# Optimization experiments

Measured on AMD Instinct MI355X. Metric: run time of the kernel, lower is better.

The kernel has to match this reference:

```python
import jax, jax.numpy as jnp
import numpy as np
from jax import lax

TRAJ_STEPS = 50  # output_dim=100 -> 50 (x,y) waypoints


def setup_inputs() -> dict:
    key = jax.random.key(0)
    ks = jax.random.split(key, 12)
    s = 0.05  # small init scale to keep gates out of saturation
    return {
        "x": jax.random.normal(ks[0], (32768, 256), jnp.float32),
        "W1": jax.random.normal(ks[1], (256, 64), jnp.float32) * s,
        "b1": jax.random.normal(ks[2], (64,), jnp.float32) * s,
        "W2": jax.random.normal(ks[3], (64, 64), jnp.float32) * s,
        "b2": jax.random.normal(ks[4], (64,), jnp.float32) * s,
        "Wih": jax.random.normal(ks[5], (2, 192), jnp.float32) * s,   # GRU input weights, gate order (r,z,n)
        "bih": jax.random.normal(ks[6], (192,), jnp.float32) * s,
        "Whh": jax.random.normal(ks[7], (64, 192), jnp.float32) * s,  # GRU hidden weights
        "bhh": jax.random.normal(ks[8], (192,), jnp.float32) * s,
        "Wout": jax.random.normal(ks[9], (64, 2), jnp.float32) * s,
        "bout": jax.random.normal(ks[10], (2,), jnp.float32) * s,
    }


def _forward(x, W1, b1, W2, b2, Wih, bih, Whh, bhh, Wout, bout):
    H = W2.shape[1]
    # backbone MLP -> initial hidden state
    z = jax.nn.relu(x @ W1 + b1)
    z = jax.nn.relu(z @ W2 + b2)  # [B, H]

    def step(carry, _):
        wp, h = carry                      # wp: [B,2] current waypoint, h: [B,H]
        gi = wp @ Wih + bih                # [B, 3H]
        gh = h @ Whh + bhh                 # [B, 3H]
        ir, iz, inn = gi[..., :H], gi[..., H:2 * H], gi[..., 2 * H:]
        hr, hz, hn = gh[..., :H], gh[..., H:2 * H], gh[..., 2 * H:]
        r = jax.nn.sigmoid(ir + hr)
        u = jax.nn.sigmoid(iz + hz)
        n = jnp.tanh(inn + r * hn)
        h_new = (1.0 - u) * n + u * h      # PyTorch GRUCell update
        dx = jax.nn.sigmoid(h_new @ Wout + bout)  # [B,2]
        wp_new = wp + dx                   # residual accumulation
        return (wp_new, h_new), wp_new

    wp0 = jnp.zeros(x.shape[:-1] + (2,), z.dtype)
    _, wps = lax.scan(step, (wp0, z), None, length=TRAJ_STEPS)  # [T, B, 2]
    wps = jnp.moveaxis(wps, 0, -2)                              # [B, T, 2]
    return wps.reshape(x.shape[:-1] + (2 * TRAJ_STEPS,))        # [B, 2T]


def reference(x, W1, b1, W2, b2, Wih, bih, Whh, bhh, Wout, bout):
    return _forward(x, W1, b1, W2, b2, Wih, bih, Whh, bhh, Wout, bout)
```

## Files before the change

kernel.cpp:

```cpp
#include <hip/hip_runtime.h>

#define TRAJ 50

typedef __attribute__((ext_vector_type(8))) short short8;
typedef __attribute__((ext_vector_type(4))) float f32x4;

#if defined(__has_builtin)
#if __has_builtin(__builtin_amdgcn_exp2f)
#define EXP2F(x) __builtin_amdgcn_exp2f(x)
#else
#define EXP2F(x) exp2f(x)
#endif
#if __has_builtin(__builtin_amdgcn_rcpf)
#define RCPF(x) __builtin_amdgcn_rcpf(x)
#else
#define RCPF(x) (1.0f/(x))
#endif
#else
#define EXP2F(x) exp2f(x)
#define RCPF(x) (1.0f/(x))
#endif

__device__ __forceinline__ float sigm(float x){
  return RCPF(1.0f + EXP2F(-1.44269504f * x));
}
__device__ __forceinline__ float tanh_(float x){
  return 1.0f - 2.0f * RCPF(1.0f + EXP2F(2.88539008f * x));
}
__device__ __forceinline__ unsigned short f2bf(float f){
  union { float f; unsigned u; } v; v.f = f;
  unsigned u = v.u;
  u += 0x7FFFu + ((u >> 16) & 1u);
  return (unsigned short)(u >> 16);
}
__device__ __forceinline__ unsigned pk(unsigned short a, unsigned short b){
  return (unsigned)a | ((unsigned)b << 16);
}

#define MFMA16(A,B,C) __builtin_amdgcn_mfma_f32_16x16x32_bf16((A),(B),(C),0,0,0)

__global__ __launch_bounds__(256, 2) void gru_actor_kernel(
    const float* __restrict__ x,
    const float* __restrict__ W1, const float* __restrict__ b1,
    const float* __restrict__ W2, const float* __restrict__ b2,
    const float* __restrict__ Wih, const float* __restrict__ bih,
    const float* __restrict__ Whh, const float* __restrict__ bhh,
    const float* __restrict__ Wout, const float* __restrict__ bout,
    float* __restrict__ out)
{
  __shared__ __align__(16) char sm_a[32768];
  __shared__ __align__(16) char sm_w[24576];
  __shared__ float sm_b1[64];
  __shared__ float sm_b2[64];

  const int t    = threadIdx.x;
  const int row0 = blockIdx.x * 64;
  const int w    = t >> 6;
  const int l    = t & 63;
  const int lr   = l & 15;
  const int lg   = l >> 4;
  const int wrow = w * 16;
  const int myrow = wrow + lr;
  const int swz  = (myrow & 7) << 4;

  {
    const float4* xg = (const float4*)(x + (size_t)row0 * 256);
    #pragma unroll
    for (int it = 0; it < 16; ++it){
      int fi = t + it * 256;
      float4 v = xg[fi];
      int e = fi * 4;
      int row = e >> 8, col = e & 255;
      unsigned p0 = pk(f2bf(v.x), f2bf(v.y));
      unsigned p1 = pk(f2bf(v.z), f2bf(v.w));
      *(uint2*)(sm_a + row * 512 + ((col * 2) ^ ((row & 7) << 4))) = make_uint2(p0, p1);
    }
  }
  for (int n = t; n < 8192; n += 256){
    int i = n & 63, kk = n >> 6;
    *(unsigned short*)(sm_w + i * 256 + ((kk * 2) ^ ((i & 7) << 4))) = f2bf(W1[kk * 64 + i]);
  }
  for (int n = t; n < 4096; n += 256){
    int i = n & 63, kk = n >> 6;
    *(unsigned short*)(sm_w + 16384 + i * 128 + ((kk * 2) ^ ((i & 7) << 4))) = f2bf(W2[kk * 64 + i]);
  }
  if (t < 64){ sm_b1[t] = b1[t]; sm_b2[t] = b2[t]; }
  __syncthreads();

  f32x4 accL[4];
  #pragma unroll
  for (int T = 0; T < 4; ++T){
    const float4 bv = *(const float4*)(sm_b1 + 16 * T + lg * 4);
    accL[T] = (f32x4){bv.x, bv.y, bv.z, bv.w};
  }
  #pragma unroll
  for (int kb = 0; kb < 4; ++kb){
    short8 B = *(const short8*)(sm_a + myrow * 512 + ((kb * 64 + lg * 16) ^ swz));
    #pragma unroll
    for (int T = 0; T < 4; ++T){
      int ai = 16 * T + lr;
      short8 A = *(const short8*)(sm_w + ai * 256 + ((kb * 64 + lg * 16) ^ ((ai & 7) << 4)));
      accL[T] = MFMA16(A, B, accL[T]);
    }
  }
  __syncthreads();
  for (int n = t; n < 8192; n += 256){
    int i = n & 63, kk = n >> 6;
    *(unsigned short*)(sm_w + i * 256 + ((kk * 2) ^ ((i & 7) << 4))) = f2bf(W1[(128 + kk) * 64 + i]);
  }
  __syncthreads();
  #pragma unroll
  for (int kb = 0; kb < 4; ++kb){
    short8 B = *(const short8*)(sm_a + myrow * 512 + (((kb + 4) * 64 + lg * 16) ^ swz));
    #pragma unroll
    for (int T = 0; T < 4; ++T){
      int ai = 16 * T + lr;
      short8 A = *(const short8*)(sm_w + ai * 256 + ((kb * 64 + lg * 16) ^ ((ai & 7) << 4)));
      accL[T] = MFMA16(A, B, accL[T]);
    }
  }
  __syncthreads();

  #pragma unroll
  for (int T = 0; T < 4; ++T){
    f32x4 a = accL[T];
    unsigned p0 = pk(f2bf(fmaxf(a[0],0.f)), f2bf(fmaxf(a[1],0.f)));
    unsigned p1 = pk(f2bf(fmaxf(a[2],0.f)), f2bf(fmaxf(a[3],0.f)));
    int ib = (16 * T + lg * 4) * 2;
    *(uint2*)(sm_a + myrow * 128 + (ib ^ swz)) = make_uint2(p0, p1);
  }
  f32x4 acc2[4];
  #pragma unroll
  for (int T = 0; T < 4; ++T){
    const float4 bv = *(const float4*)(sm_b2 + 16 * T + lg * 4);
    acc2[T] = (f32x4){bv.x, bv.y, bv.z, bv.w};
  }
  #pragma unroll
  for (int kb = 0; kb < 2; ++kb){
    short8 B = *(const short8*)(sm_a + myrow * 128 + ((kb * 64 + lg * 16) ^ swz));
    #pragma unroll
    for (int T = 0; T < 4; ++T){
      int ai = 16 * T + lr;
      short8 A = *(const short8*)(sm_w + 16384 + ai * 128 + ((kb * 64 + lg * 16) ^ ((ai & 7) << 4)));
      acc2[T] = MFMA16(A, B, acc2[T]);
    }
  }
  float h[16];
  #pragma unroll
  for (int T = 0; T < 4; ++T){
    f32x4 a = acc2[T];
    #pragma unroll
    for (int r = 0; r < 4; ++r) h[4*T+r] = fmaxf(a[r], 0.f);
    unsigned p0 = pk(f2bf(h[4*T+0]), f2bf(h[4*T+1]));
    unsigned p1 = pk(f2bf(h[4*T+2]), f2bf(h[4*T+3]));
    int ib = (16 * T + lg * 4) * 2;
    *(uint2*)(sm_a + myrow * 128 + (ib ^ swz)) = make_uint2(p0, p1);
  }
  __syncthreads();

  for (int n = t; n < 12288; n += 256){
    int kk = n / 192;
    int i  = n - kk * 192;
    *(unsigned short*)(sm_w + i * 128 + ((kk * 2) ^ ((i & 7) << 4))) = f2bf(Whh[kk * 192 + i]);
  }
  __syncthreads();

  short8 Ah[12][2];
  #pragma unroll
  for (int T = 0; T < 12; ++T){
    int i = 16 * T + lr;
    #pragma unroll
    for (int kb = 0; kb < 2; ++kb)
      Ah[T][kb] = *(const short8*)(sm_w + i * 128 + ((kb * 64 + lg * 16) ^ ((i & 7) << 4)));
  }
  short8 Ak2[16];
  #pragma unroll
  for (int T = 0; T < 16; ++T){
    short8 f = (short8){0,0,0,0,0,0,0,0};
    if (lg == 0){
      float v0 = 0.f, v1 = 0.f, v2 = 0.f;
      if (T < 8){ int i = 16*T + lr; v0 = Wih[i]; v1 = Wih[192 + i]; v2 = bih[i] + bhh[i]; }
      else if (T < 12){ int i = 16*T + lr; v2 = bhh[i]; }
      else { int i = 128 + 16*(T-12) + lr; v0 = Wih[i]; v1 = Wih[192 + i]; v2 = bih[i]; }
      f[0] = (short)f2bf(v0); f[1] = (short)f2bf(v1); f[2] = (short)f2bf(v2);
    }
    Ak2[T] = f;
  }
  short8 Aout[2];
  #pragma unroll
  for (int kb = 0; kb < 2; ++kb){
    short8 f = (short8){0,0,0,0,0,0,0,0};
    if (lr < 2){
      #pragma unroll
      for (int j = 0; j < 8; ++j){
        int k = kb * 32 + lg * 8 + j;
        f[j] = (short)f2bf(Wout[k * 2 + lr]);
      }
    }
    Aout[kb] = f;
  }
  const float bo0 = bout[0], bo1 = bout[1];

  float wp0 = 0.f, wp1 = 0.f;
  float* outp = out + (size_t)(row0 + myrow) * 100;

  short8 B0 = *(const short8*)(sm_a + myrow * 128 + ((lg * 16) ^ swz));
  short8 B1 = *(const short8*)(sm_a + myrow * 128 + ((64 + lg * 16) ^ swz));

  #pragma unroll 1
  for (int s = 0; s < TRAJ; ++s){
    short8 B2 = (short8){0,0,0,0,0,0,0,0};
    if (lg == 0){
      B2[0] = (short)f2bf(wp0);
      B2[1] = (short)f2bf(wp1);
      B2[2] = (short)0x3F80;
    }
    #pragma unroll
    for (int tq = 0; tq < 4; ++tq){
      f32x4 aR = (f32x4){0,0,0,0}, aU = (f32x4){0,0,0,0};
      f32x4 aN = (f32x4){0,0,0,0}, aI = (f32x4){0,0,0,0};
      aR = MFMA16(Ah[tq    ][0], B0, aR);
      aR = MFMA16(Ah[tq    ][1], B1, aR);
      aR = MFMA16(Ak2[tq    ],   B2, aR);
      aU = MFMA16(Ah[4 + tq][0], B0, aU);
      aU = MFMA16(Ah[4 + tq][1], B1, aU);
      aU = MFMA16(Ak2[4 + tq],   B2, aU);
      aN = MFMA16(Ah[8 + tq][0], B0, aN);
      aN = MFMA16(Ah[8 + tq][1], B1, aN);
      aN = MFMA16(Ak2[8 + tq],   B2, aN);
      aI = MFMA16(Ak2[12 + tq],  B2, aI);
      #pragma unroll
      for (int r = 0; r < 4; ++r){
        float rv = sigm(aR[r]);
        float uv = sigm(aU[r]);
        float nv = tanh_(aI[r] + rv * aN[r]);
        int idx = 4 * tq + r;
        h[idx] = (1.f - uv) * nv + uv * h[idx];
      }
      unsigned p0 = pk(f2bf(h[4*tq+0]), f2bf(h[4*tq+1]));
      unsigned p1 = pk(f2bf(h[4*tq+2]), f2bf(h[4*tq+3]));
      *(uint2*)(sm_a + myrow * 128 + (((16*tq + lg*4)*2) ^ swz)) = make_uint2(p0, p1);
    }
    short8 nB0 = *(const short8*)(sm_a + myrow * 128 + ((lg * 16) ^ swz));
    short8 nB1 = *(const short8*)(sm_a + myrow * 128 + ((64 + lg * 16) ^ swz));
    f32x4 aD = (f32x4){0,0,0,0};
    if (lg == 0){ aD[0] = bo0; aD[1] = bo1; }
    aD = MFMA16(Aout[0], nB0, aD);
    aD = MFMA16(Aout[1], nB1, aD);
    if (lg == 0){
      wp0 += sigm(aD[0]);
      wp1 += sigm(aD[1]);
      *(float2*)(outp + 2 * s) = make_float2(wp0, wp1);
    }
    B0 = nB0; B1 = nB1;
  }
}

extern "C" void kernel_launch(void* const* d_in, const int* in_sizes, int n_in,
                              void* d_out, int out_size, void* d_ws, size_t ws_size,
                              hipStream_t stream) {
  (void)n_in; (void)out_size; (void)d_ws; (void)ws_size;
  const float* x    = (const float*)d_in[0];
  const float* W1   = (const float*)d_in[1];
  const float* b1   = (const float*)d_in[2];
  const float* W2   = (const float*)d_in[3];
  const float* b2   = (const float*)d_in[4];
  const float* Wih  = (const float*)d_in[5];
  const float* bih  = (const float*)d_in[6];
  const float* Whh  = (const float*)d_in[7];
  const float* bhh  = (const float*)d_in[8];
  const float* Wout = (const float*)d_in[9];
  const float* bout = (const float*)d_in[10];
  float* out = (float*)d_out;

  int nrows = in_sizes[0] / 256;
  int grid  = nrows / 64;
  gru_actor_kernel<<<dim3(grid), dim3(256), 0, stream>>>(
      x, W1, b1, W2, b2, Wih, bih, Whh, bhh, Wout, bout, out);
}
```

Baseline: 121.7 us.

## Split GRU gate columns across wave pairs with double-buffered hidden state

Block size doubles to 512 threads and each pair of waves shares 16 rows, with each wave computing half of the hidden units. The hidden state is exchanged through a double-buffered LDS region, with a block barrier every step. The sigmoid and tanh scale factors are folded into the weights, and the two sigmoids share a single reciprocal. W1 is now staged whole in LDS instead of in two halves. The aim is to halve the per-wave serial MFMA and transcendental chain in the 50-step recurrence and to drop register pressure, at the cost of a __syncthreads per step and more LDS per block.

```diff
diff --git a/kernel.cpp b/kernel.cpp
--- a/kernel.cpp
+++ b/kernel.cpp
@@ -1,4 +1,5 @@
 #include <hip/hip_runtime.h>
+#include <hip/hip_bf16.h>
 
 #define TRAJ 50
 
@@ -21,12 +22,6 @@
 #define RCPF(x) (1.0f/(x))
 #endif
 
-__device__ __forceinline__ float sigm(float x){
-  return RCPF(1.0f + EXP2F(-1.44269504f * x));
-}
-__device__ __forceinline__ float tanh_(float x){
-  return 1.0f - 2.0f * RCPF(1.0f + EXP2F(2.88539008f * x));
-}
 __device__ __forceinline__ unsigned short f2bf(float f){
   union { float f; unsigned u; } v; v.f = f;
   unsigned u = v.u;
@@ -36,10 +31,23 @@
 __device__ __forceinline__ unsigned pk(unsigned short a, unsigned short b){
   return (unsigned)a | ((unsigned)b << 16);
 }
+__device__ __forceinline__ unsigned pkbf(float a, float b){
+  union { __hip_bfloat162 h; unsigned u; } c;
+  c.h = __float22bfloat162_rn(make_float2(a, b));
+  return c.u;
+}
+__device__ __forceinline__ short8 mkfrag(uint2 v){
+  union { unsigned u[4]; short8 s; } c;
+  c.u[0] = v.x; c.u[1] = v.y; c.u[2] = 0u; c.u[3] = 0u;
+  return c.s;
+}
 
 #define MFMA16(A,B,C) __builtin_amdgcn_mfma_f32_16x16x32_bf16((A),(B),(C),0,0,0)
 
-__global__ __launch_bounds__(256, 2) void gru_actor_kernel(
+#define SSC (-1.44269504f)
+#define TSC ( 2.88539008f)
+
+__global__ __launch_bounds__(512, 4) void gru_actor_kernel(
     const float* __restrict__ x,
     const float* __restrict__ W1, const float* __restrict__ b1,
     const float* __restrict__ W2, const float* __restrict__ b2,
@@ -48,209 +56,198 @@
     const float* __restrict__ Wout, const float* __restrict__ bout,
     float* __restrict__ out)
 {
-  __shared__ __align__(16) char sm_a[32768];
-  __shared__ __align__(16) char sm_w[24576];
+  __shared__ __align__(16) char sm_x[32768];
+  __shared__ __align__(16) char sm_w[32768];
+  __shared__ __align__(16) char sm_w2[8192];
+  __shared__ __align__(16) char sm_wo[2048];
   __shared__ float sm_b1[64];
   __shared__ float sm_b2[64];
 
   const int t    = threadIdx.x;
   const int row0 = blockIdx.x * 64;
   const int w    = t >> 6;
+  const int pair = w >> 1;
+  const int p    = w & 1;
   const int l    = t & 63;
   const int lr   = l & 15;
   const int lg   = l >> 4;
-  const int wrow = w * 16;
-  const int myrow = wrow + lr;
-  const int swz  = (myrow & 7) << 4;
+  const int myrow = pair * 16 + lr;
+  const int swz  = (lr & 7) << 4;
 
   {
     const float4* xg = (const float4*)(x + (size_t)row0 * 256);
     #pragma unroll
-    for (int it = 0; it < 16; ++it){
-      int fi = t + it * 256;
+    for (int it = 0; it < 8; ++it){
+      int fi = t + it * 512;
       float4 v = xg[fi];
-      int e = fi * 4;
-      int row = e >> 8, col = e & 255;
-      unsigned p0 = pk(f2bf(v.x), f2bf(v.y));
-      unsigned p1 = pk(f2bf(v.z), f2bf(v.w));
-      *(uint2*)(sm_a + row * 512 + ((col * 2) ^ ((row & 7) << 4))) = make_uint2(p0, p1);
-    }
-  }
-  for (int n = t; n < 8192; n += 256){
+      int e = fi * 4, row = e >> 8, col = e & 255;
+      *(uint2*)(sm_x + row * 512 + ((col * 2) ^ ((row & 7) << 4))) =
+          make_uint2(pkbf(v.x, v.y), pkbf(v.z, v.w));
+    }
+  }
+  for (int n = t; n < 16384; n += 512){
     int i = n & 63, kk = n >> 6;
-    *(unsigned short*)(sm_w + i * 256 + ((kk * 2) ^ ((i & 7) << 4))) = f2bf(W1[kk * 64 + i]);
-  }
-  for (int n = t; n < 4096; n += 256){
+    *(unsigned short*)(sm_w + i * 512 + ((kk * 2) ^ ((i & 7) << 4))) = f2bf(W1[kk * 64 + i]);
+  }
+  for (int n = t; n < 4096; n += 512){
     int i = n & 63, kk = n >> 6;
-    *(unsigned short*)(sm_w + 16384 + i * 128 + ((kk * 2) ^ ((i & 7) << 4))) = f2bf(W2[kk * 64 + i]);
+    *(unsigned short*)(sm_w2 + i * 128 + ((kk * 2) ^ ((i & 7) << 4))) = f2bf(W2[kk * 64 + i]);
+  }
+  for (int n = t; n < 1024; n += 512){
+    int row = n & 15, k = n >> 4;
+    float v = (row < 2) ? SSC * Wout[k * 2 + row] : 0.0f;
+    *(unsigned short*)(sm_wo + row * 128 + k * 2) = f2bf(v);
   }
   if (t < 64){ sm_b1[t] = b1[t]; sm_b2[t] = b2[t]; }
   __syncthreads();
 
-  f32x4 accL[4];
+  const int ar0 = 16 * (2 * p + 0) + lr;
+  const int ar1 = 16 * (2 * p + 1) + lr;
+  f32x4 accL0, accL1;
+  {
+    float4 bva = *(const float4*)(sm_b1 + 16 * (2 * p + 0) + lg * 4);
+    float4 bvb = *(const float4*)(sm_b1 + 16 * (2 * p + 1) + lg * 4);
+    accL0 = (f32x4){bva.x, bva.y, bva.z, bva.w};
+    accL1 = (f32x4){bvb.x, bvb.y, bvb.z, bvb.w};
+  }
   #pragma unroll
-  for (int T = 0; T < 4; ++T){
-    const float4 bv = *(const float4*)(sm_b1 + 16 * T + lg * 4);
-    accL[T] = (f32x4){bv.x, bv.y, bv.z, bv.w};
-  }
+  for (int kb = 0; kb < 8; ++kb){
+    short8 B  = *(const short8*)(sm_x + myrow * 512 + ((kb * 64 + lg * 16) ^ swz));
+    short8 Aa = *(const short8*)(sm_w + ar0 * 512 + ((kb * 64 + lg * 16) ^ swz));
+    short8 Ab = *(const short8*)(sm_w + ar1 * 512 + ((kb * 64 + lg * 16) ^ swz));
+    accL0 = MFMA16(Aa, B, accL0);
+    accL1 = MFMA16(Ab, B, accL1);
+  }
+  __syncthreads();
+
+  {
+    f32x4 a0 = accL0, a1 = accL1;
+    *(uint2*)(sm_x + myrow * 128 + ((64 * p + 0  + 8 * lg) ^ swz)) =
+        make_uint2(pkbf(fmaxf(a0[0],0.f), fmaxf(a0[1],0.f)), pkbf(fmaxf(a0[2],0.f), fmaxf(a0[3],0.f)));
+    *(uint2*)(sm_x + myrow * 128 + ((64 * p + 32 + 8 * lg) ^ swz)) =
+        make_uint2(pkbf(fmaxf(a1[0],0.f), fmaxf(a1[1],0.f)), pkbf(fmaxf(a1[2],0.f), fmaxf(a1[3],0.f)));
+  }
+  for (int n = t; n < 12288; n += 512){
+    int kk = n / 192, i = n - kk * 192;
+    float s = (i < 128) ? SSC : TSC;
+    *(unsigned short*)(sm_w + i * 128 + ((kk * 2) ^ ((i & 7) << 4))) = f2bf(s * Whh[kk * 192 + i]);
+  }
+  __syncthreads();
+
+  float h[8];
+  {
+    f32x4 acc20, acc21;
+    float4 bva = *(const float4*)(sm_b2 + 16 * (2 * p + 0) + lg * 4);
+    float4 bvb = *(const float4*)(sm_b2 + 16 * (2 * p + 1) + lg * 4);
+    acc20 = (f32x4){bva.x, bva.y, bva.z, bva.w};
+    acc21 = (f32x4){bvb.x, bvb.y, bvb.z, bvb.w};
+    #pragma unroll
+    for (int kb = 0; kb < 2; ++kb){
+      short8 B  = *(const short8*)(sm_x + myrow * 128 + ((kb * 64 + lg * 16) ^ swz));
+      short8 Aa = *(const short8*)(sm_w2 + ar0 * 128 + ((kb * 64 + lg * 16) ^ swz));
+      short8 Ab = *(const short8*)(sm_w2 + ar1 * 128 + ((kb * 64 + lg * 16) ^ swz));
+      acc20 = MFMA16(Aa, B, acc20);
+      acc21 = MFMA16(Ab, B, acc21);
+    }
+    #pragma unroll
+    for (int r = 0; r < 4; ++r){ h[r] = fmaxf(acc20[r], 0.f); h[4 + r] = fmaxf(acc21[r], 0.f); }
+    *(uint2*)(sm_x + 8192 + myrow * 128 + ((64 * p + 0  + 8 * lg) ^ swz)) =
+        make_uint2(pkbf(h[0], h[1]), pkbf(h[2], h[3]));
+    *(uint2*)(sm_x + 8192 + myrow * 128 + ((64 * p + 32 + 8 * lg) ^ swz)) =
+        make_uint2(pkbf(h[4], h[5]), pkbf(h[6], h[7]));
+  }
+
+  short8 Ah[3][2][2];
   #pragma unroll
-  for (int kb = 0; kb < 4; ++kb){
-    short8 B = *(const short8*)(sm_a + myrow * 512 + ((kb * 64 + lg * 16) ^ swz));
-    #pragma unroll
-    for (int T = 0; T < 4; ++T){
-      int ai = 16 * T + lr;
-      short8 A = *(const short8*)(sm_w + ai * 256 + ((kb * 64 + lg * 16) ^ ((ai & 7) << 4)));
-      accL[T] = MFMA16(A, B, accL[T]);
-    }
-  }
-  __syncthreads();
-  for (int n = t; n < 8192; n += 256){
-    int i = n & 63, kk = n >> 6;
-    *(unsigned short*)(sm_w + i * 256 + ((kk * 2) ^ ((i & 7) << 4))) = f2bf(W1[(128 + kk) * 64 + i]);
-  }
-  __syncthreads();
-  #pragma unroll
-  for (int kb = 0; kb < 4; ++kb){
-    short8 B = *(const short8*)(sm_a + myrow * 512 + (((kb + 4) * 64 + lg * 16) ^ swz));
-    #pragma unroll
-    for (int T = 0; T < 4; ++T){
-      int ai = 16 * T + lr;
-      short8 A = *(const short8*)(sm_w + ai * 256 + ((kb * 64 + lg * 16) ^ ((ai & 7) << 4)));
-      accL[T] = MFMA16(A, B, accL[T]);
-    }
-  }
-  __syncthreads();
-
-  #pragma unroll
-  for (int T = 0; T < 4; ++T){
-    f32x4 a = accL[T];
-    unsigned p0 = pk(f2bf(fmaxf(a[0],0.f)), f2bf(fmaxf(a[1],0.f)));
-    unsigned p1 = pk(f2bf(fmaxf(a[2],0.f)), f2bf(fmaxf(a[3],0.f)));
-    int ib = (16 * T + lg * 4) * 2;
-    *(uint2*)(sm_a + myrow * 128 + (ib ^ swz)) = make_uint2(p0, p1);
-  }
-  f32x4 acc2[4];
-  #pragma unroll
-  for (int T = 0; T < 4; ++T){
-    const float4 bv = *(const float4*)(sm_b2 + 16 * T + lg * 4);
-    acc2[T] = (f32x4){bv.x, bv.y, bv.z, bv.w};
-  }
-  #pragma unroll
-  for (int kb = 0; kb < 2; ++kb){
-    short8 B = *(const short8*)(sm_a + myrow * 128 + ((kb * 64 + lg * 16) ^ swz));
-    #pragma unroll
-    for (int T = 0; T < 4; ++T){
-      int ai = 16 * T + lr;
-      short8 A = *(const short8*)(sm_w + 16384 + ai * 128 + ((kb * 64 + lg * 16) ^ ((ai & 7) << 4)));
-      acc2[T] = MFMA16(A, B, acc2[T]);
-    }
-  }
-  float h[16];
-  #pragma unroll
-  for (int T = 0; T < 4; ++T){
-    f32x4 a = acc2[T];
-    #pragma unroll
-    for (int r = 0; r < 4; ++r) h[4*T+r] = fmaxf(a[r], 0.f);
-    unsigned p0 = pk(f2bf(h[4*T+0]), f2bf(h[4*T+1]));
-    unsigned p1 = pk(f2bf(h[4*T+2]), f2bf(h[4*T+3]));
-    int ib = (16 * T + lg * 4) * 2;
-    *(uint2*)(sm_a + myrow * 128 + (ib ^ swz)) = make_uint2(p0, p1);
-  }
-  __syncthreads();
-
-  for (int n = t; n < 12288; n += 256){
-    int kk = n / 192;
-    int i  = n - kk * 192;
-    *(unsigned short*)(sm_w + i * 128 + ((kk * 2) ^ ((i & 7) << 4))) = f2bf(Whh[kk * 192 + i]);
-  }
-  __syncthreads();
-
-  short8 Ah[12][2];
-  #pragma unroll
-  for (int T = 0; T < 12; ++T){
-    int i = 16 * T + lr;
-    #pragma unroll
-    for (int kb = 0; kb < 2; ++kb)
-      Ah[T][kb] = *(const short8*)(sm_w + i * 128 + ((kb * 64 + lg * 16) ^ ((i & 7) << 4)));
-  }
-  short8 Ak2[16];
-  #pragma unroll
-  for (int T = 0; T < 16; ++T){
-    short8 f = (short8){0,0,0,0,0,0,0,0};
-    if (lg == 0){
-      float v0 = 0.f, v1 = 0.f, v2 = 0.f;
-      if (T < 8){ int i = 16*T + lr; v0 = Wih[i]; v1 = Wih[192 + i]; v2 = bih[i] + bhh[i]; }
-      else if (T < 12){ int i = 16*T + lr; v2 = bhh[i]; }
-      else { int i = 128 + 16*(T-12) + lr; v0 = Wih[i]; v1 = Wih[192 + i]; v2 = bih[i]; }
-      f[0] = (short)f2bf(v0); f[1] = (short)f2bf(v1); f[2] = (short)f2bf(v2);
-    }
-    Ak2[T] = f;
-  }
-  short8 Aout[2];
-  #pragma unroll
-  for (int kb = 0; kb < 2; ++kb){
-    short8 f = (short8){0,0,0,0,0,0,0,0};
-    if (lr < 2){
+  for (int g = 0; g < 3; ++g){
+    #pragma unroll
+    for (int tql = 0; tql < 2; ++tql){
+      int i = g * 64 + 32 * p + 16 * tql + lr;
       #pragma unroll
-      for (int j = 0; j < 8; ++j){
-        int k = kb * 32 + lg * 8 + j;
-        f[j] = (short)f2bf(Wout[k * 2 + lr]);
-      }
-    }
-    Aout[kb] = f;
-  }
-  const float bo0 = bout[0], bo1 = bout[1];
+      for (int kb = 0; kb < 2; ++kb)
+        Ah[g][tql][kb] = *(const short8*)(sm_w + i * 128 + ((kb * 64 + lg * 16) ^ swz));
+    }
+  }
+  uint2 Ak2p[4][2] = {};
+  if (lg == 0){
+    #pragma unroll
+    for (int tql = 0; tql < 2; ++tql){
+      int dr = 32 * p + 16 * tql + lr;
+      int du = 64 + dr, dn = 128 + dr;
+      Ak2p[0][tql] = make_uint2(pk(f2bf(SSC*Wih[dr]), f2bf(SSC*Wih[192+dr])),
+                                pk(f2bf(SSC*(bih[dr]+bhh[dr])), 0));
+      Ak2p[1][tql] = make_uint2(pk(f2bf(SSC*Wih[du]), f2bf(SSC*Wih[192+du])),
+                                pk(f2bf(SSC*(bih[du]+bhh[du])), 0));
+      Ak2p[2][tql] = make_uint2(0u, pk(f2bf(TSC*bhh[dn]), 0));
+      Ak2p[3][tql] = make_uint2(pk(f2bf(TSC*Wih[dn]), f2bf(TSC*Wih[192+dn])),
+                                pk(f2bf(TSC*bih[dn]), 0));
+    }
+  }
+  const float bo0 = SSC * bout[0], bo1 = SSC * bout[1];
+  __syncthreads();
 
   float wp0 = 0.f, wp1 = 0.f;
   float* outp = out + (size_t)(row0 + myrow) * 100;
-
-  short8 B0 = *(const short8*)(sm_a + myrow * 128 + ((lg * 16) ^ swz));
-  short8 B1 = *(const short8*)(sm_a + myrow * 128 + ((64 + lg * 16) ^ swz));
+  short8 B0 = *(const short8*)(sm_x + 8192 + myrow * 128 + ((0  + lg * 16) ^ swz));
+  short8 B1 = *(const short8*)(sm_x + 8192 + myrow * 128 + ((64 + lg * 16) ^ swz));
 
   #pragma unroll 1
   for (int s = 0; s < TRAJ; ++s){
-    short8 B2 = (short8){0,0,0,0,0,0,0,0};
-    if (lg == 0){
-      B2[0] = (short)f2bf(wp0);
-      B2[1] = (short)f2bf(wp1);
-      B2[2] = (short)0x3F80;
-    }
-    #pragma unroll
-    for (int tq = 0; tq < 4; ++tq){
+    char* bufW = sm_x + ((s & 1) << 13);
+    short8 B2;
+    {
+      unsigned b2lo = 0u, b2hi = 0u;
+      if (lg == 0){ b2lo = pkbf(wp0, wp1); b2hi = 0x00003F80u; }
+      union { unsigned u[4]; short8 sv; } c;
+      c.u[0] = b2lo; c.u[1] = b2hi; c.u[2] = 0u; c.u[3] = 0u;
+      B2 = c.sv;
+    }
+    #pragma unroll
+    for (int tql = 0; tql < 2; ++tql){
       f32x4 aR = (f32x4){0,0,0,0}, aU = (f32x4){0,0,0,0};
       f32x4 aN = (f32x4){0,0,0,0}, aI = (f32x4){0,0,0,0};
-      aR = MFMA16(Ah[tq    ][0], B0, aR);
-      aR = MFMA16(Ah[tq    ][1], B1, aR);
-      aR = MFMA16(Ak2[tq    ],   B2, aR);
-      aU = MFMA16(Ah[4 + tq][0], B0, aU);
-      aU = MFMA16(Ah[4 + tq][1], B1, aU);
-      aU = MFMA16(Ak2[4 + tq],   B2, aU);
-      aN = MFMA16(Ah[8 + tq][0], B0, aN);
-      aN = MFMA16(Ah[8 + tq][1], B1, aN);
-      aN = MFMA16(Ak2[8 + tq],   B2, aN);
-      aI = MFMA16(Ak2[12 + tq],  B2, aI);
+      aR = MFMA16(Ah[0][tql][0], B0, aR);
+      aR = MFMA16(Ah[0][tql][1], B1, aR);
+      aR = MFMA16(mkfrag(Ak2p[0][tql]), B2, aR);
+      aU = MFMA16(Ah[1][tql][0], B0, aU);
+      aU = MFMA16(Ah[1][tql][1], B1, aU);
+      aU = MFMA16(mkfrag(Ak2p[1][tql]), B2, aU);
+      aN = MFMA16(Ah[2][tql][0], B0, aN);
+      aN = MFMA16(Ah[2][tql][1], B1, aN);
+      aN = MFMA16(mkfrag(Ak2p[2][tql]), B2, aN);
+      aI = MFMA16(mkfrag(Ak2p[3][tql]), B2, aI);
       #pragma unroll
       for (int r = 0; r < 4; ++r){
-        float rv = sigm(aR[r]);
-        float uv = sigm(aU[r]);
-        float nv = tanh_(aI[r] + rv * aN[r]);
-        int idx = 4 * tq + r;
-        h[idx] = (1.f - uv) * nv + uv * h[idx];
+        float e1 = EXP2F(aR[r]);
+        float e2 = EXP2F(aU[r]);
+        float d1 = 1.f + e1, d2 = 1.f + e2;
+        float rp = RCPF(d1 * d2);
+        float rv = d2 * rp;
+        float uv = d1 * rp;
+        float y  = fmaf(rv, aN[r], aI[r]);
+        float nv = fmaf(-2.f, RCPF(1.f + EXP2F(y)), 1.f);
+        int hi_ = 4 * tql + r;
+        h[hi_] = fmaf(uv, h[hi_] - nv, nv);
       }
-      unsigned p0 = pk(f2bf(h[4*tq+0]), f2bf(h[4*tq+1]));
-      unsigned p1 = pk(f2bf(h[4*tq+2]), f2bf(h[4*tq+3]));
-      *(uint2*)(sm_a + myrow * 128 + (((16*tq + lg*4)*2) ^ swz)) = make_uint2(p0, p1);
-    }
-    short8 nB0 = *(const short8*)(sm_a + myrow * 128 + ((lg * 16) ^ swz));
-    short8 nB1 = *(const short8*)(sm_a + myrow * 128 + ((64 + lg * 16) ^ swz));
+      *(uint2*)(bufW + myrow * 128 + ((64 * p + 32 * tql + 8 * lg) ^ swz)) =
+          make_uint2(pkbf(h[4*tql+0], h[4*tql+1]), pkbf(h[4*tql+2], h[4*tql+3]));
+    }
+    __syncthreads();
+    short8 nB0 = *(const short8*)(bufW + myrow * 128 + ((0  + lg * 16) ^ swz));
+    short8 nB1 = *(const short8*)(bufW + myrow * 128 + ((64 + lg * 16) ^ swz));
+    short8 Ao0 = *(const short8*)(sm_wo + lr * 128 + 0  + lg * 16);
+    short8 Ao1 = *(const short8*)(sm_wo + lr * 128 + 64 + lg * 16);
     f32x4 aD = (f32x4){0,0,0,0};
     if (lg == 0){ aD[0] = bo0; aD[1] = bo1; }
-    aD = MFMA16(Aout[0], nB0, aD);
-    aD = MFMA16(Aout[1], nB1, aD);
+    aD = MFMA16(Ao0, nB0, aD);
+    aD = MFMA16(Ao1, nB1, aD);
     if (lg == 0){
-      wp0 += sigm(aD[0]);
-      wp1 += sigm(aD[1]);
-      *(float2*)(outp + 2 * s) = make_float2(wp0, wp1);
+      float ea = EXP2F(aD[0]), eb = EXP2F(aD[1]);
+      float da = 1.f + ea, db = 1.f + eb;
+      float rp = RCPF(da * db);
+      wp0 += db * rp;
+      wp1 += da * rp;
+      if (p == 0) *(float2*)(outp + 2 * s) = make_float2(wp0, wp1);
     }
     B0 = nB0; B1 = nB1;
   }
@@ -275,6 +272,6 @@
 
   int nrows = in_sizes[0] / 256;
   int grid  = nrows / 64;
-  gru_actor_kernel<<<dim3(grid), dim3(256), 0, stream>>>(
+  gru_actor_kernel<<<dim3(grid), dim3(512), 0, stream>>>(
       x, W1, b1, W2, b2, Wih, bih, Whh, bhh, Wout, bout, out);
 }
```

Measured after the change: 117.7 us. 3.3% less time.
